# Performance work log

Hardware: AMD Instinct MI355X
Metric: run time of the kernel (lower is better)

## Reference

```python
import jax, jax.numpy as jnp
import numpy as np

A, B, D, L = 256, 64, 768, 2  # annotators, batch, hidden, num_labels
G1, G2 = 4, 8                 # groups per attribute


def setup_inputs() -> dict:
    key = jax.random.key(0)
    ks = jax.random.split(key, 9)
    s = 1.0 / np.sqrt(D)
    return {
        "pooled": jax.random.normal(ks[0], (B, D), jnp.float32),
        "W1": jax.random.normal(ks[1], (G1, D, D), jnp.float32) * s,
        "b1": jax.random.normal(ks[2], (G1, D), jnp.float32) * s,
        "W2": jax.random.normal(ks[3], (G2, D, D), jnp.float32) * s,
        "b2": jax.random.normal(ks[4], (G2, D), jnp.float32) * s,
        "Wh": jax.random.normal(ks[5], (A, D, L), jnp.float32) * s,
        "bh": jax.random.normal(ks[6], (A, L), jnp.float32) * s,
        "g1_idx": jax.random.randint(ks[7], (A,), 0, G1),
        "g2_idx": jax.random.randint(ks[8], (A,), 0, G2),
    }


def reference(pooled, W1, b1, W2, b2, Wh, bh, g1_idx, g2_idx):
    # Attribute 1: every annotator with the same group shares the transform,
    # so compute once per group then gather (avoids A redundant GEMMs).
    h_g = jnp.einsum('bd,gde->gbe', pooled, W1) + b1[:, None, :]   # [G1, B, D]
    h = h_g[g1_idx]                                                # [A, B, D]
    # Attribute 2: input now differs per annotator -> grouped GEMM via gathered weights.
    h = jnp.einsum('abd,ade->abe', h, W2[g2_idx]) + b2[g2_idx][:, None, :]  # [A, B, D]
    # Per-annotator classification heads.
    logits = jnp.einsum('abd,adl->abl', h, Wh) + bh[:, None, :]    # [A, B, L]
    # Match torch layout: logits[batch, annotator, label]
    return jnp.transpose(logits, (1, 0, 2))                        # [B, A, L]
```

## Files before the change

kernel.cpp:

```cpp
#include <hip/hip_runtime.h>

#define AN 256
#define BN 64
#define DN 768
#define LN 2
#define G1N 4
#define G2N 8
#define KI (DN / 32)
#define PAD 776

typedef __attribute__((ext_vector_type(8))) short short8;
typedef __attribute__((ext_vector_type(4))) short bf16x4;
typedef __attribute__((ext_vector_type(4))) float floatx4;

static __device__ __forceinline__ unsigned short f2bf(float f) {
    union { float f; unsigned int u; } v; v.f = f;
    unsigned int r = v.u + 0x7FFF + ((v.u >> 16) & 1);
    return (unsigned short)(r >> 16);
}
static __device__ __forceinline__ unsigned int pack2(float a, float b) {
    return (unsigned int)f2bf(a) | ((unsigned int)f2bf(b) << 16);
}

__global__ __launch_bounds__(256) void k_main(
    const float* __restrict__ pooled, const float* __restrict__ W1,
    const float* __restrict__ b1, const float* __restrict__ W2,
    const float* __restrict__ b2, const float* __restrict__ Wh,
    const float* __restrict__ bh, const int* __restrict__ g2i,
    unsigned short* __restrict__ h1, unsigned short* __restrict__ Wcs,
    float* __restrict__ bc)
{
    __shared__ __align__(16) unsigned char smem[64 * PAD * 2];
    const int tid = threadIdx.x, bx = blockIdx.x;
    const int lane = tid & 63, wave = tid >> 6;
    const int nn = lane & 15, quad = lane >> 4;

    if (bx < 48) {
        unsigned short* ps = (unsigned short*)smem;
        {
            const float4* p4 = (const float4*)pooled;
            #pragma unroll
            for (int i = 0; i < 48; ++i) {
                const int idx = i * 256 + tid;
                float4 v = p4[idx];
                const int row = idx / 192, c4 = idx % 192;
                const unsigned long long w =
                    (unsigned long long)pack2(v.x, v.y) |
                    ((unsigned long long)pack2(v.z, v.w) << 32);
                *(unsigned long long*)(ps + row * PAD + c4 * 4) = w;
            }
        }
        __syncthreads();

        const int g = bx / 12, e0 = (bx % 12) * 64;
        const int e = e0 + wave * 16 + nn;
        const float* Wcol = W1 + (size_t)g * DN * DN + e;
        const unsigned short* Ap = ps + nn * PAD + quad * 8;
        floatx4 acc[4] = {{0,0,0,0},{0,0,0,0},{0,0,0,0},{0,0,0,0}};
        #pragma unroll
        for (int kk = 0; kk < KI; ++kk) {
            const float* wk = Wcol + (size_t)(kk * 32 + quad * 8) * DN;
            short8 bf;
            #pragma unroll
            for (int j = 0; j < 8; ++j)
                bf[j] = (short)f2bf(wk[(size_t)j * DN]);
            #pragma unroll
            for (int mt = 0; mt < 4; ++mt) {
                short8 af = *(const short8*)(Ap + (mt * 16) * PAD + kk * 32);
                acc[mt] = __builtin_amdgcn_mfma_f32_16x16x32_bf16(af, bf, acc[mt], 0, 0, 0);
            }
        }
        const float bv = b1[g * DN + e];
        #pragma unroll
        for (int mt = 0; mt < 4; ++mt)
            #pragma unroll
            for (int r = 0; r < 4; ++r)
                h1[(size_t)g * BN * DN + (size_t)(mt * 16 + quad * 4 + r) * DN + e] =
                    f2bf(acc[mt][r] + bv);
    } else if (bx < 144) {
        int* g2s  = (int*)smem;
        int* lst2 = (int*)(smem + 1024);
        unsigned short* Whs = (unsigned short*)(smem + 2048);

        const int j = bx - 48, g = j / 12, mbase = (j % 12) * 64;

        const int m_row = mbase + wave * 16 + nn;
        const float* ap = W2 + ((size_t)g * DN + m_row) * DN + quad * 8;
        short8 Areg[KI];
        #pragma unroll
        for (int kk = 0; kk < KI; ++kk) {
            float4 a0 = *(const float4*)(ap + kk * 32);
            float4 a1 = *(const float4*)(ap + kk * 32 + 4);
            short8 af;
            af[0] = (short)f2bf(a0.x); af[1] = (short)f2bf(a0.y);
            af[2] = (short)f2bf(a0.z); af[3] = (short)f2bf(a0.w);
            af[4] = (short)f2bf(a1.x); af[5] = (short)f2bf(a1.y);
            af[6] = (short)f2bf(a1.z); af[7] = (short)f2bf(a1.w);
            Areg[kk] = af;
        }

        g2s[tid] = g2i[tid];
        __syncthreads();
        const int my = g2s[tid];
        int rk = 0;
        for (int a2 = 0; a2 < tid; ++a2) rk += (g2s[a2] == my);
        if (my == g) lst2[rk] = tid;
        int n2g = 0;
        for (int a2 = 0; a2 < AN; ++a2) n2g += (g2s[a2] == g);
        __syncthreads();
        const int cols = 2 * n2g;

        const int al = tid >> 5, t32 = tid & 31;
        for (int c0 = 0; c0 < cols; c0 += 16) {
            const int sidx = (c0 >> 1) + al;
            if (sidx < n2g) {
                const int a = lst2[sidx];
                const float4* wa4 = (const float4*)(Wh + (size_t)a * (DN * LN));
                #pragma unroll
                for (int i = 0; i < 12; ++i) {
                    const int f4 = i * 32 + t32;
                    float4 v = wa4[f4];
                    const int e2 = f4 * 2;
                    *(unsigned int*)(Whs + (2 * al)     * PAD + e2) = pack2(v.x, v.z);
                    *(unsigned int*)(Whs + (2 * al + 1) * PAD + e2) = pack2(v.y, v.w);
                }
            }
            __syncthreads();
            const unsigned short* Brow = Whs + nn * PAD + quad * 8;
            floatx4 acc = {0, 0, 0, 0};
            #pragma unroll
            for (int kk = 0; kk < KI; ++kk) {
                short8 bf = *(const short8*)(Brow + kk * 32);
                acc = __builtin_amdgcn_mfma_f32_16x16x32_bf16(Areg[kk], bf, acc, 0, 0, 0);
            }
            const int c = c0 + nn;
            if (c < cols) {
                const int dbase = mbase + wave * 16 + quad * 4;
                bf16x4 v;
                #pragma unroll
                for (int r = 0; r < 4; ++r) v[r] = (short)f2bf(acc[r]);
                *(bf16x4*)(Wcs + (size_t)(g * 256 + c) * DN + dbase) = v;
            }
            __syncthreads();
        }
    } else {
        const int jb = bx - 144;
        const int aa = tid >> 3, jj = tid & 7;
        const int a = jb * 32 + aa;
        const int gv2 = g2i[a];
        const float* whp = Wh + (size_t)a * (DN * LN);
        const float* b2p = b2 + gv2 * DN;
        float acc0 = 0.f, acc1 = 0.f;
        #pragma unroll 4
        for (int i = 0; i < 48; ++i) {
            int e = jj * 96 + i * 2;
            float4 w4 = *(const float4*)(whp + e * 2);
            float2 bv = *(const float2*)(b2p + e);
            acc0 += bv.x * w4.x + bv.y * w4.z;
            acc1 += bv.x * w4.y + bv.y * w4.w;
        }
        #pragma unroll
        for (int off = 4; off; off >>= 1) {
            acc0 += __shfl_down(acc0, off, 64);
            acc1 += __shfl_down(acc1, off, 64);
        }
        if (jj == 0) {
            bc[a * 2 + 0] = acc0 + bh[a * 2 + 0];
            bc[a * 2 + 1] = acc1 + bh[a * 2 + 1];
        }
    }
}

__global__ __launch_bounds__(256) void k_out(
    const unsigned short* __restrict__ h1, const unsigned short* __restrict__ Wcs,
    const float* __restrict__ bc, const int* __restrict__ g1i,
    const int* __restrict__ g2i, float* __restrict__ out)
{
    __shared__ int g1s[AN], g2s[AN], lst1[AN], sx2[AN];
    const int g = blockIdx.y;
    const int tid = threadIdx.x;
    g1s[tid] = g1i[tid];
    g2s[tid] = g2i[tid];
    __syncthreads();
    const int m1 = g1s[tid], m2 = g2s[tid];
    int r1 = 0, r2 = 0;
    for (int a2 = 0; a2 < tid; ++a2) {
        r1 += (g1s[a2] == m1);
        r2 += (g2s[a2] == m2);
    }
    sx2[tid] = r2;
    if (m1 == g) lst1[r1] = tid;
    int n1g = 0;
    for (int a2 = 0; a2 < AN; ++a2) n1g += (g1s[a2] == g);
    __syncthreads();

    const int cols = 2 * n1g;
    const int nt0 = blockIdx.x * 16;
    if (nt0 >= cols) return;

    const int lane = tid & 63, wave = tid >> 6;
    const int nn = lane & 15, quad = lane >> 4;

    const int c = nt0 + nn;
    const bool valid = (c < cols);
    const int cl = valid ? c : (cols - 1);
    const int a = lst1[cl >> 1];
    const int l = cl & 1;
    const int rp = (g2s[a] * 128 + sx2[a]) * 2 + l;

    const unsigned short* hg = h1 + (size_t)g * BN * DN + (size_t)(wave * 16 + nn) * DN + quad * 8;
    const unsigned short* wp = Wcs + (size_t)rp * DN + quad * 8;

    floatx4 acc = {0, 0, 0, 0};
    #pragma unroll
    for (int kk = 0; kk < KI; ++kk) {
        short8 af = *(const short8*)(hg + kk * 32);
        short8 bf = *(const short8*)(wp + kk * 32);
        acc = __builtin_amdgcn_mfma_f32_16x16x32_bf16(af, bf, acc, 0, 0, 0);
    }
    if (valid) {
        const float bv = bc[a * 2 + l];
        #pragma unroll
        for (int r = 0; r < 4; ++r)
            out[(size_t)(wave * 16 + quad * 4 + r) * (AN * LN) + a * 2 + l] = acc[r] + bv;
    }
}

extern "C" void kernel_launch(void* const* d_in, const int* in_sizes, int n_in,
                              void* d_out, int out_size, void* d_ws, size_t ws_size,
                              hipStream_t stream) {
    const float* pooled = (const float*)d_in[0];
    const float* W1     = (const float*)d_in[1];
    const float* b1     = (const float*)d_in[2];
    const float* W2     = (const float*)d_in[3];
    const float* b2     = (const float*)d_in[4];
    const float* Wh     = (const float*)d_in[5];
    const float* bh     = (const float*)d_in[6];
    const int*   g1i    = (const int*)d_in[7];
    const int*   g2i    = (const int*)d_in[8];
    float* out = (float*)d_out;

    char* ws = (char*)d_ws;
    float* bc = (float*)ws;                           ws += 512 * 4;
    unsigned short* h1  = (unsigned short*)ws;        ws += (size_t)G1N * BN * DN * 2;
    unsigned short* Wcs = (unsigned short*)ws;

    dim3 blk(256);
    k_main<<<dim3(152),   blk, 0, stream>>>(pooled, W1, b1, W2, b2, Wh, bh, g2i,
                                            h1, Wcs, bc);
    k_out <<<dim3(32, 4), blk, 0, stream>>>(h1, Wcs, bc, g1i, g2i, out);
}
```

Before: 116.4 us.

## Fuse producer and output kernels into one launch with global-memory flags

Merges the two kernel launches into one 256-block kernel. The producer blocks (h1 GEMM, Wcs GEMM, bias fold) publish completion by storing a magic value to per-block flags after a thread fence. The 104 consumer blocks spin on the flags they depend on, then run the final grouped MFMA output work, taking one or two jobs each. This removes the launch boundary and lets output tiles start as soon as their inputs are ready. It relies on all 256 blocks being resident at once, and the flags are never reset between calls, so later calls can pass the wait on stale flags and race with the producers.

```diff
diff --git a/kernel.cpp b/kernel.cpp
--- a/kernel.cpp
+++ b/kernel.cpp
@@ -8,6 +8,7 @@
 #define G2N 8
 #define KI (DN / 32)
 #define PAD 776
+#define MAGIC 0x5F3C9A71
 
 typedef __attribute__((ext_vector_type(8))) short short8;
 typedef __attribute__((ext_vector_type(4))) short bf16x4;
@@ -21,14 +22,23 @@
 static __device__ __forceinline__ unsigned int pack2(float a, float b) {
     return (unsigned int)f2bf(a) | ((unsigned int)f2bf(b) << 16);
 }
-
-__global__ __launch_bounds__(256) void k_main(
+static __device__ __forceinline__ void sig_flag(int* f) {
+    __hip_atomic_store(f, MAGIC, __ATOMIC_RELAXED, __HIP_MEMORY_SCOPE_AGENT);
+}
+static __device__ __forceinline__ void wait_flag(int* f) {
+    while (__hip_atomic_load(f, __ATOMIC_RELAXED, __HIP_MEMORY_SCOPE_AGENT) != MAGIC)
+        __builtin_amdgcn_s_sleep(2);
+}
+
+__global__ __launch_bounds__(256) void k_all(
     const float* __restrict__ pooled, const float* __restrict__ W1,
     const float* __restrict__ b1, const float* __restrict__ W2,
     const float* __restrict__ b2, const float* __restrict__ Wh,
-    const float* __restrict__ bh, const int* __restrict__ g2i,
+    const float* __restrict__ bh, const int* __restrict__ g1i,
+    const int* __restrict__ g2i,
     unsigned short* __restrict__ h1, unsigned short* __restrict__ Wcs,
-    float* __restrict__ bc)
+    float* __restrict__ bc, int* __restrict__ flags,
+    float* __restrict__ out)
 {
     __shared__ __align__(16) unsigned char smem[64 * PAD * 2];
     const int tid = threadIdx.x, bx = blockIdx.x;
@@ -77,6 +87,9 @@
             for (int r = 0; r < 4; ++r)
                 h1[(size_t)g * BN * DN + (size_t)(mt * 16 + quad * 4 + r) * DN + e] =
                     f2bf(acc[mt][r] + bv);
+
+        __syncthreads();
+        if (tid == 0) { __threadfence(); sig_flag(&flags[bx]); }
     } else if (bx < 144) {
         int* g2s  = (int*)smem;
         int* lst2 = (int*)(smem + 1024);
@@ -143,7 +156,10 @@
             }
             __syncthreads();
         }
-    } else {
+
+        __syncthreads();
+        if (tid == 0) { __threadfence(); sig_flag(&flags[bx]); }
+    } else if (bx < 152) {
         const int jb = bx - 144;
         const int aa = tid >> 3, jj = tid & 7;
         const int a = jb * 32 + aa;
@@ -168,61 +184,72 @@
             bc[a * 2 + 0] = acc0 + bh[a * 2 + 0];
             bc[a * 2 + 1] = acc1 + bh[a * 2 + 1];
         }
-    }
-}
-
-__global__ __launch_bounds__(256) void k_out(
-    const unsigned short* __restrict__ h1, const unsigned short* __restrict__ Wcs,
-    const float* __restrict__ bc, const int* __restrict__ g1i,
-    const int* __restrict__ g2i, float* __restrict__ out)
-{
-    __shared__ int g1s[AN], g2s[AN], lst1[AN], sx2[AN];
-    const int g = blockIdx.y;
-    const int tid = threadIdx.x;
-    g1s[tid] = g1i[tid];
-    g2s[tid] = g2i[tid];
-    __syncthreads();
-    const int m1 = g1s[tid], m2 = g2s[tid];
-    int r1 = 0, r2 = 0;
-    for (int a2 = 0; a2 < tid; ++a2) {
-        r1 += (g1s[a2] == m1);
-        r2 += (g2s[a2] == m2);
-    }
-    sx2[tid] = r2;
-    if (m1 == g) lst1[r1] = tid;
-    int n1g = 0;
-    for (int a2 = 0; a2 < AN; ++a2) n1g += (g1s[a2] == g);
-    __syncthreads();
-
-    const int cols = 2 * n1g;
-    const int nt0 = blockIdx.x * 16;
-    if (nt0 >= cols) return;
-
-    const int lane = tid & 63, wave = tid >> 6;
-    const int nn = lane & 15, quad = lane >> 4;
-
-    const int c = nt0 + nn;
-    const bool valid = (c < cols);
-    const int cl = valid ? c : (cols - 1);
-    const int a = lst1[cl >> 1];
-    const int l = cl & 1;
-    const int rp = (g2s[a] * 128 + sx2[a]) * 2 + l;
-
-    const unsigned short* hg = h1 + (size_t)g * BN * DN + (size_t)(wave * 16 + nn) * DN + quad * 8;
-    const unsigned short* wp = Wcs + (size_t)rp * DN + quad * 8;
-
-    floatx4 acc = {0, 0, 0, 0};
-    #pragma unroll
-    for (int kk = 0; kk < KI; ++kk) {
-        short8 af = *(const short8*)(hg + kk * 32);
-        short8 bf = *(const short8*)(wp + kk * 32);
-        acc = __builtin_amdgcn_mfma_f32_16x16x32_bf16(af, bf, acc, 0, 0, 0);
-    }
-    if (valid) {
-        const float bv = bc[a * 2 + l];
-        #pragma unroll
-        for (int r = 0; r < 4; ++r)
-            out[(size_t)(wave * 16 + quad * 4 + r) * (AN * LN) + a * 2 + l] = acc[r] + bv;
+        __syncthreads();
+        if (tid == 0) { __threadfence(); sig_flag(&flags[bx]); }
+    } else {
+        int* g1s  = (int*)smem;
+        int* g2s  = (int*)(smem + 1024);
+        int* lst1 = (int*)(smem + 2048);
+        int* sx2  = (int*)(smem + 3072);
+
+        const int j0 = bx - 152;
+        const int njobs = (j0 < 24) ? 2 : 1;
+        for (int ji = 0; ji < njobs; ++ji) {
+            const int job = j0 + ji * 104;
+            const int g = job >> 5;
+
+            if (tid < 96)       wait_flag(&flags[48 + tid]);
+            else if (tid < 104) wait_flag(&flags[144 + (tid - 96)]);
+            else if (tid < 116) wait_flag(&flags[g * 12 + (tid - 104)]);
+            __syncthreads();
+            __threadfence();
+
+            g1s[tid] = g1i[tid];
+            g2s[tid] = g2i[tid];
+            __syncthreads();
+            const int m1 = g1s[tid], m2 = g2s[tid];
+            int r1 = 0, r2 = 0;
+            for (int a2 = 0; a2 < tid; ++a2) {
+                r1 += (g1s[a2] == m1);
+                r2 += (g2s[a2] == m2);
+            }
+            sx2[tid] = r2;
+            if (m1 == g) lst1[r1] = tid;
+            int n1g = 0;
+            for (int a2 = 0; a2 < AN; ++a2) n1g += (g1s[a2] == g);
+            __syncthreads();
+
+            const int cols = 2 * n1g;
+            const int nt0 = (job & 31) * 16;
+            if (nt0 < cols) {
+                const int c = nt0 + nn;
+                const bool valid = (c < cols);
+                const int cl = valid ? c : (cols - 1);
+                const int a = lst1[cl >> 1];
+                const int l = cl & 1;
+                const int rp = (g2s[a] * 128 + sx2[a]) * 2 + l;
+
+                const unsigned short* hg = h1 + (size_t)g * BN * DN
+                                              + (size_t)(wave * 16 + nn) * DN + quad * 8;
+                const unsigned short* wp = Wcs + (size_t)rp * DN + quad * 8;
+
+                floatx4 acc = {0, 0, 0, 0};
+                #pragma unroll
+                for (int kk = 0; kk < KI; ++kk) {
+                    short8 af = *(const short8*)(hg + kk * 32);
+                    short8 bf = *(const short8*)(wp + kk * 32);
+                    acc = __builtin_amdgcn_mfma_f32_16x16x32_bf16(af, bf, acc, 0, 0, 0);
+                }
+                if (valid) {
+                    const float bv = bc[a * 2 + l];
+                    #pragma unroll
+                    for (int r = 0; r < 4; ++r)
+                        out[(size_t)(wave * 16 + quad * 4 + r) * (AN * LN) + a * 2 + l] =
+                            acc[r] + bv;
+                }
+            }
+            __syncthreads();
+        }
     }
 }
 
@@ -241,12 +268,11 @@
     float* out = (float*)d_out;
 
     char* ws = (char*)d_ws;
-    float* bc = (float*)ws;                           ws += 512 * 4;
+    int*   flags = (int*)ws;                          ws += 256 * 4;
+    float* bc    = (float*)ws;                        ws += 512 * 4;
     unsigned short* h1  = (unsigned short*)ws;        ws += (size_t)G1N * BN * DN * 2;
     unsigned short* Wcs = (unsigned short*)ws;
 
-    dim3 blk(256);
-    k_main<<<dim3(152),   blk, 0, stream>>>(pooled, W1, b1, W2, b2, Wh, bh, g2i,
-                                            h1, Wcs, bc);
-    k_out <<<dim3(32, 4), blk, 0, stream>>>(h1, Wcs, bc, g1i, g2i, out);
-}
+    k_all<<<dim3(256), dim3(256), 0, stream>>>(pooled, W1, b1, W2, b2, Wh, bh,
+                                               g1i, g2i, h1, Wcs, bc, flags, out);
+}
```

Result: slower. 138.9 us (+19.3%).

## Split W1 GEMM into narrower tiles with double-buffered LDS staging of W1

Applied to the files above, without the earlier changes.

Each block of the first GEMM now handles 16 output columns instead of 64, so that phase launches 192 blocks instead of 48 and the grid grows to 296. W1 tiles are staged through a padded, double-buffered LDS region with a prefetch of the next k-slice, replacing strided per-lane global loads. Each wave now loads pooled directly from global memory and converts it to bf16 per iteration instead of reading a shared bf16 copy. This trades more total pooled traffic and a barrier per k-step for higher parallelism and coalesced W1 loads.

```diff
diff --git a/kernel.cpp b/kernel.cpp
--- a/kernel.cpp
+++ b/kernel.cpp
@@ -30,59 +30,68 @@
     unsigned short* __restrict__ h1, unsigned short* __restrict__ Wcs,
     float* __restrict__ bc)
 {
-    __shared__ __align__(16) unsigned char smem[64 * PAD * 2];
+    __shared__ __align__(16) unsigned char smem[26880];
     const int tid = threadIdx.x, bx = blockIdx.x;
     const int lane = tid & 63, wave = tid >> 6;
     const int nn = lane & 15, quad = lane >> 4;
 
-    if (bx < 48) {
-        unsigned short* ps = (unsigned short*)smem;
+    if (bx < 192) {
+        float* ldsW = (float*)smem;
+        const int g = bx / 48, e0 = (bx % 48) * 16;
+        const float* src = W1 + (size_t)g * DN * DN + e0;
+        const int r = tid >> 3, c2 = (tid & 7) * 2;
+
         {
-            const float4* p4 = (const float4*)pooled;
-            #pragma unroll
-            for (int i = 0; i < 48; ++i) {
-                const int idx = i * 256 + tid;
-                float4 v = p4[idx];
-                const int row = idx / 192, c4 = idx % 192;
-                const unsigned long long w =
-                    (unsigned long long)pack2(v.x, v.y) |
-                    ((unsigned long long)pack2(v.z, v.w) << 32);
-                *(unsigned long long*)(ps + row * PAD + c4 * 4) = w;
-            }
+            float2 v = *(const float2*)(src + (size_t)r * DN + c2);
+            float* d = ldsW + r * 17 + c2;
+            d[0] = v.x; d[1] = v.y;
         }
         __syncthreads();
 
-        const int g = bx / 12, e0 = (bx % 12) * 64;
-        const int e = e0 + wave * 16 + nn;
-        const float* Wcol = W1 + (size_t)g * DN * DN + e;
-        const unsigned short* Ap = ps + nn * PAD + quad * 8;
-        floatx4 acc[4] = {{0,0,0,0},{0,0,0,0},{0,0,0,0},{0,0,0,0}};
-        #pragma unroll
+        const int mt = wave;
+        const float* Ap = pooled + (size_t)(mt * 16 + nn) * DN + quad * 8;
+        floatx4 acc = {0, 0, 0, 0};
         for (int kk = 0; kk < KI; ++kk) {
-            const float* wk = Wcol + (size_t)(kk * 32 + quad * 8) * DN;
+            const int cur = kk & 1;
+            float2 vnext;
+            if (kk + 1 < KI)
+                vnext = *(const float2*)(src + (size_t)((kk + 1) * 32 + r) * DN + c2);
+
+            const float* wb = ldsW + cur * 544 + quad * 8 * 17 + nn;
             short8 bf;
             #pragma unroll
             for (int j = 0; j < 8; ++j)
-                bf[j] = (short)f2bf(wk[(size_t)j * DN]);
-            #pragma unroll
-            for (int mt = 0; mt < 4; ++mt) {
-                short8 af = *(const short8*)(Ap + (mt * 16) * PAD + kk * 32);
-                acc[mt] = __builtin_amdgcn_mfma_f32_16x16x32_bf16(af, bf, acc[mt], 0, 0, 0);
-            }
-        }
+                bf[j] = (short)f2bf(wb[j * 17]);
+
+            float4 a0 = *(const float4*)(Ap + kk * 32);
+            float4 a1 = *(const float4*)(Ap + kk * 32 + 4);
+            short8 af;
+            af[0] = (short)f2bf(a0.x); af[1] = (short)f2bf(a0.y);
+            af[2] = (short)f2bf(a0.z); af[3] = (short)f2bf(a0.w);
+            af[4] = (short)f2bf(a1.x); af[5] = (short)f2bf(a1.y);
+            af[6] = (short)f2bf(a1.z); af[7] = (short)f2bf(a1.w);
+
+            acc = __builtin_amdgcn_mfma_f32_16x16x32_bf16(af, bf, acc, 0, 0, 0);
+
+            if (kk + 1 < KI) {
+                float* d = ldsW + (cur ^ 1) * 544 + r * 17 + c2;
+                d[0] = vnext.x; d[1] = vnext.y;
+            }
+            __syncthreads();
+        }
+
+        const int e = e0 + nn;
         const float bv = b1[g * DN + e];
         #pragma unroll
-        for (int mt = 0; mt < 4; ++mt)
-            #pragma unroll
-            for (int r = 0; r < 4; ++r)
-                h1[(size_t)g * BN * DN + (size_t)(mt * 16 + quad * 4 + r) * DN + e] =
-                    f2bf(acc[mt][r] + bv);
-    } else if (bx < 144) {
+        for (int rr = 0; rr < 4; ++rr)
+            h1[(size_t)g * BN * DN + (size_t)(mt * 16 + quad * 4 + rr) * DN + e] =
+                f2bf(acc[rr] + bv);
+    } else if (bx < 288) {
         int* g2s  = (int*)smem;
         int* lst2 = (int*)(smem + 1024);
         unsigned short* Whs = (unsigned short*)(smem + 2048);
 
-        const int j = bx - 48, g = j / 12, mbase = (j % 12) * 64;
+        const int j = bx - 192, g = j / 12, mbase = (j % 12) * 64;
 
         const int m_row = mbase + wave * 16 + nn;
         const float* ap = W2 + ((size_t)g * DN + m_row) * DN + quad * 8;
@@ -138,13 +147,13 @@
                 const int dbase = mbase + wave * 16 + quad * 4;
                 bf16x4 v;
                 #pragma unroll
-                for (int r = 0; r < 4; ++r) v[r] = (short)f2bf(acc[r]);
+                for (int rr = 0; rr < 4; ++rr) v[rr] = (short)f2bf(acc[rr]);
                 *(bf16x4*)(Wcs + (size_t)(g * 256 + c) * DN + dbase) = v;
             }
             __syncthreads();
         }
     } else {
-        const int jb = bx - 144;
+        const int jb = bx - 288;
         const int aa = tid >> 3, jj = tid & 7;
         const int a = jb * 32 + aa;
         const int gv2 = g2i[a];
@@ -246,7 +255,7 @@
     unsigned short* Wcs = (unsigned short*)ws;
 
     dim3 blk(256);
-    k_main<<<dim3(152),   blk, 0, stream>>>(pooled, W1, b1, W2, b2, Wh, bh, g2i,
+    k_main<<<dim3(296),   blk, 0, stream>>>(pooled, W1, b1, W2, b2, Wh, bh, g2i,
                                             h1, Wcs, bc);
     k_out <<<dim3(32, 4), blk, 0, stream>>>(h1, Wcs, bc, g1i, g2i, out);
 }
```

Measured after the change: 131.2 us. 1.13x slower.
